# Kernel optimization log

Hardware: AMD Instinct MI355X
Metric: run time of the kernel (lower is better)

Reference implementation:

```python
import jax, jax.numpy as jnp
import numpy as np

D_MODEL = 768; N_LAYERS = 12; D_STATE = 128; D_CONV = 4; HEADDIM = 64
D_INNER = 2 * D_MODEL            # 1536
NHEADS = D_INNER // HEADDIM      # 24
CONV_DIM = D_INNER + 2 * D_STATE # 1792
D_IN_PROJ = 2 * D_INNER + 2 * D_STATE + NHEADS  # 3352
D_FF = 2048; VOCAB = 32000; BATCH = 2; SEQ = 2048
EPS = 1e-5


def setup_inputs() -> dict:
    key = jax.random.key(0)
    ks = jax.random.split(key, 20)
    s = 0.02
    inp = {
        'input_ids': jax.random.randint(ks[0], (BATCH, SEQ), 0, VOCAB),
        'emb':    jax.random.normal(ks[1], (VOCAB, D_MODEL)) * s,
        'ln_w':   jnp.ones((N_LAYERS, D_MODEL)),
        'ln_b':   jnp.zeros((N_LAYERS, D_MODEL)),
        'in_w':   jax.random.normal(ks[2], (N_LAYERS, D_IN_PROJ, D_MODEL)) * s,
        'conv_w': jax.random.normal(ks[3], (N_LAYERS, CONV_DIM, D_CONV)) * 0.1,
        'conv_b': jnp.zeros((N_LAYERS, CONV_DIM)),
        'dt_bias': jax.random.normal(ks[4], (N_LAYERS, NHEADS)) * 0.5,
        'A_log':  jnp.log(1.0 + jax.random.uniform(ks[5], (N_LAYERS, NHEADS)) * 15.0),
        'Dp':     jnp.ones((N_LAYERS, NHEADS)),
        'rms_w':  jnp.ones((N_LAYERS, D_INNER)),
        'out_w':  jax.random.normal(ks[6], (N_LAYERS, D_MODEL, D_INNER)) * s,
        'mlp_ln_w': jnp.ones((N_LAYERS, D_MODEL)),
        'mlp_ln_b': jnp.zeros((N_LAYERS, D_MODEL)),
        'w1':     jax.random.normal(ks[7], (N_LAYERS, D_FF, D_MODEL)) * s,
        'w2':     jax.random.normal(ks[8], (N_LAYERS, D_FF, D_MODEL)) * s,
        'w3':     jax.random.normal(ks[9], (N_LAYERS, D_MODEL, D_FF)) * s,
        'normf_w': jnp.ones((D_MODEL,)),
        'normf_b': jnp.zeros((D_MODEL,)),
        'lm_w':   jax.random.normal(ks[10], (VOCAB, D_MODEL)) * s,
    }
    return inp


def layer_norm(x, w, b):
    mu = jnp.mean(x, -1, keepdims=True)
    xc = x - mu
    var = jnp.mean(xc * xc, -1, keepdims=True)
    return xc * jax.lax.rsqrt(var + EPS) * w + b


def mamba_mixer(h, in_w, conv_w, conv_b, dt_bias, A_log, Dp, rms_w, out_w):
    b, l, _ = h.shape
    zxbcdt = jnp.einsum('bld,ed->ble', h, in_w)                 # [b,l,3352]
    z = zxbcdt[..., :D_INNER]
    xBC = zxbcdt[..., D_INNER:D_INNER + CONV_DIM]
    dt = jax.nn.softplus(zxbcdt[..., D_INNER + CONV_DIM:] + dt_bias)  # [b,l,nh]
    # causal depthwise conv1d over time, kernel D_CONV, then silu
    xpad = jnp.pad(xBC, ((0, 0), (D_CONV - 1, 0), (0, 0)))
    conv = conv_b
    for k in range(D_CONV):
        conv = conv + conv_w[:, k] * xpad[:, k:k + l, :]
    xBC = jax.nn.silu(conv)
    x = xBC[..., :D_INNER].reshape(b, l, NHEADS, HEADDIM)
    Bm = xBC[..., D_INNER:D_INNER + D_STATE]                    # [b,l,n] (ngroups=1)
    Cm = xBC[..., D_INNER + D_STATE:]                           # [b,l,n]
    A = -jnp.exp(A_log)                                         # [nh]
    dA = jnp.exp(dt * A)                                        # [b,l,nh]
    dtB = dt[..., None] * Bm[:, :, None, :]                     # [b,l,nh,n]

    def step(state, inputs):
        dA_t, dtB_t, x_t, C_t = inputs
        state = state * dA_t[..., None, None] + dtB_t[:, :, None, :] * x_t[..., None]
        y_t = jnp.einsum('bhpn,bn->bhp', state, C_t)
        return state, y_t

    state0 = jnp.zeros((b, NHEADS, HEADDIM, D_STATE), dtype=h.dtype)
    xs = (jnp.moveaxis(dA, 1, 0), jnp.moveaxis(dtB, 1, 0),
          jnp.moveaxis(x, 1, 0), jnp.moveaxis(Cm, 1, 0))
    _, ys = jax.lax.scan(step, state0, xs)
    y = jnp.moveaxis(ys, 0, 1) + Dp[None, None, :, None] * x    # [b,l,nh,hd]
    y = y.reshape(b, l, D_INNER)
    # gated RMSNorm (norm_before_gate=False)
    y = y * jax.nn.silu(z)
    y = y * jax.lax.rsqrt(jnp.mean(y * y, -1, keepdims=True) + EPS) * rms_w
    return jnp.einsum('ble,de->bld', y, out_w)


def reference(input_ids, emb, ln_w, ln_b, in_w, conv_w, conv_b, dt_bias, A_log, Dp,
              rms_w, out_w, mlp_ln_w, mlp_ln_b, w1, w2, w3, normf_w, normf_b, lm_w):
    h = emb[input_ids]                                          # [b,l,d]
    for i in range(N_LAYERS):
        resid = h
        hn = layer_norm(resid, ln_w[i], ln_b[i])
        hm = mamba_mixer(hn, in_w[i], conv_w[i], conv_b[i], dt_bias[i],
                         A_log[i], Dp[i], rms_w[i], out_w[i])
        hf = hm + resid
        g = layer_norm(hf, mlp_ln_w[i], mlp_ln_b[i])
        h = hf + jnp.einsum('blf,df->bld', jax.nn.silu(jnp.einsum('bld,fd->blf', g, w1[i])) *
                            jnp.einsum('bld,fd->blf', g, w2[i]), w3[i])
    h = layer_norm(h, normf_w, normf_b)
    return jnp.einsum('bld,vd->blv', h, lm_w)
```

## Files before the change

### kernel.cpp

```cpp
#include <hip/hip_runtime.h>
#include <cstdint>
#include <cstddef>

#define TOK    4096
#define SEQL   2048
#define DMODEL 768
#define NLAYER 12
#define DSTATE 128
#define HEADD  64
#define DINNER 1536
#define NHEADS 24
#define CONVD  1792
#define DIPROJ 3352
#define DIPAD  3456
#define DFF    2048
#define VOCABN 32000
#define NCHUNK 16
#define CHUNKL 128

typedef __attribute__((ext_vector_type(8))) short bf16x8;
typedef __attribute__((ext_vector_type(4))) float f32x4;

__device__ __forceinline__ unsigned short f2bf(float f) {
  union { float f; unsigned u; } v; v.f = f;
  return (unsigned short)((v.u + 0x7FFFu + ((v.u >> 16) & 1u)) >> 16);
}

__device__ __forceinline__ void gld16(const void* g, void* l) {
  __builtin_amdgcn_global_load_lds(
      (const __attribute__((address_space(1))) unsigned int*)g,
      (__attribute__((address_space(3))) unsigned int*)l, 16, 0, 0);
}

__device__ __forceinline__ void stream_store(float* addr, float v) {
  asm volatile("global_store_dword %0, %1, off sc0 sc1 nt" :: "v"(addr), "v"(v) : "memory");
}

template <int NW>
__device__ __forceinline__ void red2t(float& a, float& b) {
#pragma unroll
  for (int o = 1; o < 64; o <<= 1) { a += __shfl_xor(a, o, 64); b += __shfl_xor(b, o, 64); }
  __shared__ float sa[NW], sb[NW];
  const int w = threadIdx.x >> 6;
  if ((threadIdx.x & 63) == 0) { sa[w] = a; sb[w] = b; }
  __syncthreads();
  a = sa[0]; b = sb[0];
#pragma unroll
  for (int i = 1; i < NW; ++i) { a += sa[i]; b += sb[i]; }
}

template <int NW>
__device__ __forceinline__ float red1t(float a) {
#pragma unroll
  for (int o = 1; o < 64; o <<= 1) a += __shfl_xor(a, o, 64);
  __shared__ float sa[NW];
  const int w = threadIdx.x >> 6;
  if ((threadIdx.x & 63) == 0) sa[w] = a;
  __syncthreads();
  float r = sa[0];
#pragma unroll
  for (int i = 1; i < NW; ++i) r += sa[i];
  return r;
}

template <int EPI, int BM, int BN>
__global__ __launch_bounds__(256) void gemm_bt(
    const unsigned short* __restrict__ A, const unsigned short* __restrict__ B,
    float* __restrict__ C, unsigned short* __restrict__ Cg,
    const float* __restrict__ R, int M, int N, int K) {
  constexpr int WM  = BM / 2, WN = BN / 2;
  constexpr int MFR = WM / 16, NFR = WN / 16;
  constexpr int LPS = (BM == 128 ? 2 : 1) + (BN == 128 ? 2 : 1);
  __shared__ unsigned short lA[2][BM * 32];
  __shared__ unsigned short lB[2][BN * 32];

  int lid = (int)blockIdx.x;
  {
    const int nwg = (int)gridDim.x;
    const int xcd = lid & 7;
    const int q = nwg >> 3, r = nwg & 7;
    const int b2 = (xcd < r) ? xcd * (q + 1) : r * (q + 1) + (xcd - r) * q;
    lid = b2 + (lid >> 3);
  }
  const int mtiles = M / BM;
  int m0, n0;
  if constexpr (BM == 128) {
    const int nt = (int)gridDim.x / mtiles;
    const int span = 16 * nt;
    const int g = lid / span, rem = lid % span;
    m0 = (g * 16 + (rem % 16)) * BM;
    n0 = (rem / 16) * BN;
  } else {
    m0 = (lid % mtiles) * BM;
    n0 = (lid / mtiles) * BN;
  }

  const int tid = threadIdx.x, wave = tid >> 6, lane = tid & 63;
  const int wr = (wave >> 1) * WM, wc = (wave & 1) * WN;
  const int srow = lane >> 2;
  const int scol = (((lane & 3) ^ ((lane >> 3) & 3))) * 8;
  const int rdk  = ((lane >> 4) ^ ((lane >> 1) & 3)) * 8;

  f32x4 acc[MFR][NFR];
#pragma unroll
  for (int i = 0; i < MFR; ++i)
#pragma unroll
    for (int j = 0; j < NFR; ++j) acc[i][j] = (f32x4){0.f, 0.f, 0.f, 0.f};

  const size_t arow0 = (size_t)(m0 + (BM == 128 ? wave * 32 : wave * 16) + srow) * K + scol;
  const size_t brow0 = (size_t)(n0 + (BN == 128 ? wave * 32 : wave * 16) + srow) * K + scol;

  auto stage = [&](int buf, int k0) {
    if constexpr (BM == 128) {
      gld16(A + arow0 + k0,                  lA[buf] + (wave * 2 + 0) * 512);
      gld16(A + arow0 + (size_t)16 * K + k0, lA[buf] + (wave * 2 + 1) * 512);
    } else {
      gld16(A + arow0 + k0, lA[buf] + wave * 512);
    }
    if constexpr (BN == 128) {
      gld16(B + brow0 + k0,                  lB[buf] + (wave * 2 + 0) * 512);
      gld16(B + brow0 + (size_t)16 * K + k0, lB[buf] + (wave * 2 + 1) * 512);
    } else {
      gld16(B + brow0 + k0, lB[buf] + wave * 512);
    }
  };

  stage(0, 0);
  stage(1, 32);
  int cur = 0;
  for (int k0 = 0; k0 < K; k0 += 32) {
    asm volatile("s_waitcnt vmcnt(%0)" :: "i"(LPS) : "memory");
    __builtin_amdgcn_s_barrier();
    bf16x8 af[MFR], bfr[NFR];
#pragma unroll
    for (int mi = 0; mi < MFR; ++mi) {
      const int ra = wr + mi * 16 + (lane & 15);
      af[mi] = *(const bf16x8*)&lA[cur][ra * 32 + rdk];
    }
#pragma unroll
    for (int ni = 0; ni < NFR; ++ni) {
      const int rb = wc + ni * 16 + (lane & 15);
      bfr[ni] = *(const bf16x8*)&lB[cur][rb * 32 + rdk];
    }
    asm volatile("s_waitcnt lgkmcnt(0)" ::: "memory");
    __builtin_amdgcn_sched_barrier(0);
    __builtin_amdgcn_s_barrier();
    if (k0 + 64 < K) stage(cur, k0 + 64);
    __builtin_amdgcn_sched_barrier(0);
#pragma unroll
    for (int mi = 0; mi < MFR; ++mi)
#pragma unroll
      for (int ni = 0; ni < NFR; ++ni)
        acc[mi][ni] = __builtin_amdgcn_mfma_f32_16x16x32_bf16(af[mi], bfr[ni], acc[mi][ni], 0, 0, 0);
    cur ^= 1;
  }

  const int er = (lane >> 4) * 4, ec = lane & 15;
#pragma unroll
  for (int mi = 0; mi < MFR; ++mi) {
#pragma unroll
    for (int r = 0; r < 4; ++r) {
      const size_t row = (size_t)(m0 + wr + mi * 16 + er + r);
#pragma unroll
      for (int ni = 0; ni < NFR; ++ni) {
        float v = acc[mi][ni][r];
        const int col = n0 + wc + ec + ni * 16;
        if constexpr (EPI == 2) {
          const float o = __shfl_xor(v, 1, 64);
          if ((lane & 1) == 0)
            Cg[row * DFF + (col >> 1)] = f2bf((v / (1.f + expf(-v))) * o);
        } else if constexpr (EPI == 1) {
          C[row * N + col] = v + R[row * N + col];
        } else if constexpr (EPI == 3) {
          stream_store(&C[row * N + col], v);
        } else {
          C[row * N + col] = v;
        }
      }
    }
  }
}

__global__ __launch_bounds__(256) void cvt_k(const float* __restrict__ in, unsigned short* __restrict__ out, long n) {
  const long i = ((long)blockIdx.x * 256 + threadIdx.x) * 4;
  if (i >= n) return;
  const float4 v = *(const float4*)(in + i);
  ushort4 o; o.x = f2bf(v.x); o.y = f2bf(v.y); o.z = f2bf(v.z); o.w = f2bf(v.w);
  *(ushort4*)(out + i) = o;
}

__global__ __launch_bounds__(256) void cvt_inw_k(const float* __restrict__ in, unsigned short* __restrict__ out) {
  const int row = blockIdx.x;
  const int l = row / DIPAD, n = row % DIPAD;
  unsigned short* orow = out + (size_t)row * DMODEL;
  if (n >= DIPROJ) {
    for (int c = threadIdx.x; c < DMODEL; c += 256) orow[c] = 0;
    return;
  }
  const float* irow = in + ((size_t)l * DIPROJ + n) * DMODEL;
  for (int c = threadIdx.x; c < DMODEL; c += 256) orow[c] = f2bf(irow[c]);
}

__global__ __launch_bounds__(256) void cvt_w12_k(const float* __restrict__ w1, const float* __restrict__ w2,
                                                 unsigned short* __restrict__ out) {
  const int row = blockIdx.x;
  const int l = row / (2 * DFF), rr = row % (2 * DFF);
  const int f = rr >> 1;
  const float* irow = ((rr & 1) == 0) ? (w1 + ((size_t)l * DFF + f) * DMODEL)
                                      : (w2 + ((size_t)l * DFF + f) * DMODEL);
  unsigned short* orow = out + (size_t)row * DMODEL;
  for (int c = threadIdx.x; c < DMODEL; c += 256) orow[c] = f2bf(irow[c]);
}

__global__ __launch_bounds__(192) void embed_k(const int* __restrict__ ids, const float* __restrict__ emb, float* __restrict__ h) {
  const int t = blockIdx.x;
  const float4 v = *(const float4*)(emb + (size_t)ids[t] * DMODEL + threadIdx.x * 4);
  *(float4*)(h + (size_t)t * DMODEL + threadIdx.x * 4) = v;
}

__global__ __launch_bounds__(192) void ln_k(const float* __restrict__ x, const float* __restrict__ w, const float* __restrict__ b,
                                            unsigned short* __restrict__ out) {
  const int t = blockIdx.x, c4 = threadIdx.x * 4;
  const float4 v = *(const float4*)(x + (size_t)t * DMODEL + c4);
  float s = v.x + v.y + v.z + v.w;
  float ss = v.x * v.x + v.y * v.y + v.z * v.z + v.w * v.w;
  red2t<3>(s, ss);
  const float mu = s * (1.f / DMODEL);
  const float inv = rsqrtf(ss * (1.f / DMODEL) - mu * mu + 1e-5f);
  const float4 wv = *(const float4*)(w + c4);
  const float4 bv = *(const float4*)(b + c4);
  ushort4 o;
  o.x = f2bf((v.x - mu) * inv * wv.x + bv.x);
  o.y = f2bf((v.y - mu) * inv * wv.y + bv.y);
  o.z = f2bf((v.z - mu) * inv * wv.z + bv.z);
  o.w = f2bf((v.w - mu) * inv * wv.w + bv.w);
  *(ushort4*)(out + (size_t)t * DMODEL + c4) = o;
}

__global__ __launch_bounds__(448) void conv_k(const float* __restrict__ zx, const float* __restrict__ cw, const float* __restrict__ cb,
                                              const float* __restrict__ dt_bias, const float* __restrict__ A_log,
                                              float* __restrict__ xs, float* __restrict__ Bm, float* __restrict__ Cm,
                                              float* __restrict__ dtv, float* __restrict__ dAv) {
  const int t = blockIdx.x, b = t >> 11, l = t & (SEQL - 1);
  const int c4 = threadIdx.x * 4;
  const float4 w0 = *(const float4*)(cw + c4 * 4);
  const float4 w1v = *(const float4*)(cw + c4 * 4 + 4);
  const float4 w2v = *(const float4*)(cw + c4 * 4 + 8);
  const float4 w3v = *(const float4*)(cw + c4 * 4 + 12);
  float4 a = *(const float4*)(cb + c4);
#pragma unroll
  for (int k = 0; k < 4; ++k) {
    const int ll = l + k - 3;
    if (ll >= 0) {
      const float4 xv = *(const float4*)(zx + (size_t)(b * SEQL + ll) * DIPAD + DINNER + c4);
      a.x = fmaf(((const float*)&w0)[k],  xv.x, a.x);
      a.y = fmaf(((const float*)&w1v)[k], xv.y, a.y);
      a.z = fmaf(((const float*)&w2v)[k], xv.z, a.z);
      a.w = fmaf(((const float*)&w3v)[k], xv.w, a.w);
    }
  }
  a.x = a.x / (1.f + expf(-a.x));
  a.y = a.y / (1.f + expf(-a.y));
  a.z = a.z / (1.f + expf(-a.z));
  a.w = a.w / (1.f + expf(-a.w));
  if (threadIdx.x < 384)      *(float4*)(xs + (size_t)t * DINNER + c4) = a;
  else if (threadIdx.x < 416) *(float4*)(Bm + (size_t)t * DSTATE + (c4 - DINNER)) = a;
  else                        *(float4*)(Cm + (size_t)t * DSTATE + (c4 - DINNER - DSTATE)) = a;
  if (threadIdx.x < NHEADS) {
    const int hh = threadIdx.x;
    const float xv = zx[(size_t)t * DIPAD + DINNER + CONVD + hh] + dt_bias[hh];
    const float dt = (xv > 20.f) ? xv : log1pf(expf(xv));
    dtv[t * NHEADS + hh] = dt;
    dAv[t * NHEADS + hh] = expf(-dt * expf(A_log[hh]));
  }
}

__global__ __launch_bounds__(256) void scan1_k(const float* __restrict__ xs, const float* __restrict__ Bm, const float* __restrict__ Cm,
                                               const float* __restrict__ dtv, const float* __restrict__ dAv,
                                               const float* __restrict__ Dp, float* __restrict__ y,
                                               float* __restrict__ Sloc, float* __restrict__ cumv) {
  __shared__ float lB[2][16][128];
  __shared__ float lC[2][16][128];
  __shared__ float sdA[2][16], sdt[2][16];
  const int pg = blockIdx.x, hh = blockIdx.y, z = blockIdx.z;
  const int b = z >> 4, c = z & (NCHUNK - 1);
  const int pl = threadIdx.x >> 4, ln = threadIdx.x & 15;
  const int p = pg * 16 + pl;
  const int wv = threadIdx.x >> 6, lane = threadIdx.x & 63;
  const float Dph = Dp[hh];
  const int bT = b * SEQL + c * CHUNKL;

  auto stage = [&](int buf, int t0) {
#pragma unroll
    for (int j = 0; j < 2; ++j) {
      const int pr = wv + 4 * j;
      const int row = 2 * pr + (lane >> 5);
      gld16(Bm + (size_t)(t0 + row) * DSTATE + (lane & 31) * 4, &lB[buf][2 * pr][0]);
      gld16(Cm + (size_t)(t0 + row) * DSTATE + (lane & 31) * 4, &lC[buf][2 * pr][0]);
    }
    if (threadIdx.x < 16)      sdA[buf][threadIdx.x]      = dAv[(t0 + threadIdx.x) * NHEADS + hh];
    else if (threadIdx.x < 32) sdt[buf][threadIdx.x - 16] = dtv[(t0 + threadIdx.x - 16) * NHEADS + hh];
  };

  float s0 = 0, s1 = 0, s2 = 0, s3 = 0, s4 = 0, s5 = 0, s6 = 0, s7 = 0;
  float r = 1.f;
  int cur = 0;
  stage(0, bT);
  for (int cc = 0; cc < CHUNKL; cc += 16) {
    const int t0 = bT + cc;
    __builtin_amdgcn_s_barrier();
    float xq[16];
#pragma unroll
    for (int i = 0; i < 16; ++i) xq[i] = xs[(size_t)(t0 + i) * DINNER + hh * HEADD + p];
    if (cc + 16 < CHUNKL) stage(cur ^ 1, t0 + 16);
    asm volatile("s_waitcnt vmcnt(4) lgkmcnt(0)" ::: "memory");
    __builtin_amdgcn_s_barrier();
#pragma unroll
    for (int i = 0; i < 16; ++i) {
      const float dAt = sdA[cur][i], dtt = sdt[cur][i];
      const float xdt = xq[i] * dtt;
      const float4 B0 = *(const float4*)&lB[cur][i][ln * 4];
      const float4 B1 = *(const float4*)&lB[cur][i][64 + ln * 4];
      const float4 C0 = *(const float4*)&lC[cur][i][ln * 4];
      const float4 C1 = *(const float4*)&lC[cur][i][64 + ln * 4];
      float yp;
      s0 = fmaf(s0, dAt, B0.x * xdt); yp = s0 * C0.x;
      s1 = fmaf(s1, dAt, B0.y * xdt); yp = fmaf(s1, C0.y, yp);
      s2 = fmaf(s2, dAt, B0.z * xdt); yp = fmaf(s2, C0.z, yp);
      s3 = fmaf(s3, dAt, B0.w * xdt); yp = fmaf(s3, C0.w, yp);
      s4 = fmaf(s4, dAt, B1.x * xdt); yp = fmaf(s4, C1.x, yp);
      s5 = fmaf(s5, dAt, B1.y * xdt); yp = fmaf(s5, C1.y, yp);
      s6 = fmaf(s6, dAt, B1.z * xdt); yp = fmaf(s6, C1.z, yp);
      s7 = fmaf(s7, dAt, B1.w * xdt); yp = fmaf(s7, C1.w, yp);
#pragma unroll
      for (int o = 1; o < 16; o <<= 1) yp += __shfl_xor(yp, o, 64);
      if (ln == 0) y[(size_t)(t0 + i) * DINNER + hh * HEADD + p] = fmaf(Dph, xq[i], yp);
      r *= dAt;
      if (threadIdx.x == 0) cumv[(size_t)(b * NHEADS + hh) * SEQL + (c * CHUNKL + cc + i)] = r;
    }
    cur ^= 1;
  }
  float* sp = Sloc + (((size_t)(b * NHEADS + hh) * NCHUNK + c) * HEADD + p) * DSTATE;
  *(float4*)(sp + ln * 4)      = (float4){s0, s1, s2, s3};
  *(float4*)(sp + 64 + ln * 4) = (float4){s4, s5, s6, s7};
}

__global__ __launch_bounds__(256) void scan2_k(float* __restrict__ Sloc, const float* __restrict__ cumv) {
  const int bh = blockIdx.x;
  const size_t base = (size_t)bh * NCHUNK * (HEADD * DSTATE);
  const int e0 = threadIdx.x * 32;
  float acc[32];
#pragma unroll
  for (int j = 0; j < 32; ++j) acc[j] = 0.f;
  for (int c = 1; c < NCHUNK; ++c) {
    const float Pc = cumv[(size_t)bh * SEQL + c * CHUNKL - 1];
    float* slot = Sloc + base + (size_t)(c - 1) * (HEADD * DSTATE) + e0;
#pragma unroll
    for (int j = 0; j < 32; j += 4) {
      const float4 sl = *(const float4*)(slot + j);
      acc[j]     = fmaf(Pc, acc[j],     sl.x);
      acc[j + 1] = fmaf(Pc, acc[j + 1], sl.y);
      acc[j + 2] = fmaf(Pc, acc[j + 2], sl.z);
      acc[j + 3] = fmaf(Pc, acc[j + 3], sl.w);
      *(float4*)(slot + j) = (float4){acc[j], acc[j + 1], acc[j + 2], acc[j + 3]};
    }
  }
}

__global__ __launch_bounds__(256) void scan3_k(const float* __restrict__ Cm, const float* __restrict__ cumv,
                                               const float* __restrict__ Sloc, float* __restrict__ y) {
  __shared__ float lC[2][16][128];
  __shared__ float sCum[2][16];
  const int pg = blockIdx.x, hh = blockIdx.y, z = blockIdx.z;
  const int b = z / (NCHUNK - 1), c = z % (NCHUNK - 1) + 1;
  const int pl = threadIdx.x >> 4, ln = threadIdx.x & 15;
  const int p = pg * 16 + pl;
  const int wv = threadIdx.x >> 6, lane = threadIdx.x & 63;
  const int bT = b * SEQL + c * CHUNKL;
  const float* sp = Sloc + (((size_t)(b * NHEADS + hh) * NCHUNK + (c - 1)) * HEADD + p) * DSTATE;
  const float4 sA = *(const float4*)(sp + ln * 4);
  const float4 sB = *(const float4*)(sp + 64 + ln * 4);

  auto stage = [&](int buf, int t0) {
#pragma unroll
    for (int j = 0; j < 2; ++j) {
      const int pr = wv + 4 * j;
      const int row = 2 * pr + (lane >> 5);
      gld16(Cm + (size_t)(t0 + row) * DSTATE + (lane & 31) * 4, &lC[buf][2 * pr][0]);
    }
    if (threadIdx.x < 16)
      sCum[buf][threadIdx.x] = cumv[(size_t)(b * NHEADS + hh) * SEQL + (t0 - b * SEQL) + threadIdx.x];
  };

  int cur = 0;
  stage(0, bT);
  for (int cc = 0; cc < CHUNKL; cc += 16) {
    const int t0 = bT + cc;
    __builtin_amdgcn_s_barrier();
    float yq[16];
#pragma unroll
    for (int i = 0; i < 16; ++i) yq[i] = y[(size_t)(t0 + i) * DINNER + hh * HEADD + p];
    if (cc + 16 < CHUNKL) stage(cur ^ 1, t0 + 16);
    asm volatile("s_waitcnt vmcnt(2) lgkmcnt(0)" ::: "memory");
    __builtin_amdgcn_s_barrier();
#pragma unroll
    for (int i = 0; i < 16; ++i) {
      const float4 C0 = *(const float4*)&lC[cur][i][ln * 4];
      const float4 C1 = *(const float4*)&lC[cur][i][64 + ln * 4];
      float yp = sA.x * C0.x;
      yp = fmaf(sA.y, C0.y, yp);
      yp = fmaf(sA.z, C0.z, yp);
      yp = fmaf(sA.w, C0.w, yp);
      yp = fmaf(sB.x, C1.x, yp);
      yp = fmaf(sB.y, C1.y, yp);
      yp = fmaf(sB.z, C1.z, yp);
      yp = fmaf(sB.w, C1.w, yp);
#pragma unroll
      for (int o = 1; o < 16; o <<= 1) yp += __shfl_xor(yp, o, 64);
      if (ln == 0) y[(size_t)(t0 + i) * DINNER + hh * HEADD + p] = fmaf(sCum[cur][i], yp, yq[i]);
    }
    cur ^= 1;
  }
}

__global__ __launch_bounds__(384) void grms_k(const float* __restrict__ y, const float* __restrict__ zx,
                                              const float* __restrict__ rw, unsigned short* __restrict__ out) {
  const int t = blockIdx.x, c4 = threadIdx.x * 4;
  const float4 yv = *(const float4*)(y + (size_t)t * DINNER + c4);
  const float4 zv = *(const float4*)(zx + (size_t)t * DIPAD + c4);
  float4 g;
  g.x = yv.x * (zv.x / (1.f + expf(-zv.x)));
  g.y = yv.y * (zv.y / (1.f + expf(-zv.y)));
  g.z = yv.z * (zv.z / (1.f + expf(-zv.z)));
  g.w = yv.w * (zv.w / (1.f + expf(-zv.w)));
  float ss = g.x * g.x + g.y * g.y + g.z * g.z + g.w * g.w;
  ss = red1t<6>(ss);
  const float inv = rsqrtf(ss * (1.f / DINNER) + 1e-5f);
  const float4 rv = *(const float4*)(rw + c4);
  ushort4 o;
  o.x = f2bf(g.x * inv * rv.x);
  o.y = f2bf(g.y * inv * rv.y);
  o.z = f2bf(g.z * inv * rv.z);
  o.w = f2bf(g.w * inv * rv.w);
  *(ushort4*)(out + (size_t)t * DINNER + c4) = o;
}

extern "C" void kernel_launch(void* const* d_in, const int* in_sizes, int n_in,
                              void* d_out, int out_size, void* d_ws, size_t ws_size,
                              hipStream_t stream) {
  const int*   ids      = (const int*)  d_in[0];
  const float* emb      = (const float*)d_in[1];
  const float* ln_w     = (const float*)d_in[2];
  const float* ln_b     = (const float*)d_in[3];
  const float* in_w     = (const float*)d_in[4];
  const float* conv_w   = (const float*)d_in[5];
  const float* conv_b   = (const float*)d_in[6];
  const float* dt_bias  = (const float*)d_in[7];
  const float* A_log    = (const float*)d_in[8];
  const float* Dp       = (const float*)d_in[9];
  const float* rms_w    = (const float*)d_in[10];
  const float* out_w    = (const float*)d_in[11];
  const float* mlp_ln_w = (const float*)d_in[12];
  const float* mlp_ln_b = (const float*)d_in[13];
  const float* w1       = (const float*)d_in[14];
  const float* w2       = (const float*)d_in[15];
  const float* w3       = (const float*)d_in[16];
  const float* normf_w  = (const float*)d_in[17];
  const float* normf_b  = (const float*)d_in[18];
  const float* lm_w     = (const float*)d_in[19];

  char* base = (char*)d_ws;
  size_t off = 0;
  auto alloc = [&](size_t bytes) -> char* {
    char* p = base + off;
    off += (bytes + 255) & ~(size_t)255;
    return p;
  };
  float* h             = (float*)alloc((size_t)TOK * DMODEL * 4);
  unsigned short* xn   = (unsigned short*)alloc((size_t)TOK * DMODEL * 2);
  float* zx            = (float*)alloc((size_t)TOK * DIPAD * 4);
  float* xs            = (float*)alloc((size_t)TOK * DINNER * 4);
  float* Bm            = (float*)alloc((size_t)TOK * DSTATE * 4);
  float* Cm            = (float*)alloc((size_t)TOK * DSTATE * 4);
  float* dtv           = (float*)alloc((size_t)TOK * NHEADS * 4);
  float* dAv           = (float*)alloc((size_t)TOK * NHEADS * 4);
  float* y             = (float*)alloc((size_t)TOK * DINNER * 4);
  unsigned short* ybf  = (unsigned short*)alloc((size_t)TOK * DINNER * 2);
  float* hf            = (float*)alloc((size_t)TOK * DMODEL * 4);
  unsigned short* gbf  = (unsigned short*)alloc((size_t)TOK * DMODEL * 2);
  unsigned short* gate = (unsigned short*)alloc((size_t)TOK * DFF * 2);
  float* Sloc          = (float*)alloc((size_t)2 * NHEADS * NCHUNK * HEADD * DSTATE * 4);
  float* cumv          = (float*)alloc((size_t)2 * NHEADS * SEQL * 4);
  unsigned short* inw_bf  = (unsigned short*)alloc((size_t)NLAYER * DIPAD * DMODEL * 2);
  unsigned short* outw_bf = (unsigned short*)alloc((size_t)NLAYER * DMODEL * DINNER * 2);
  unsigned short* w12_bf  = (unsigned short*)alloc((size_t)NLAYER * 2 * DFF * DMODEL * 2);
  unsigned short* w3_bf   = (unsigned short*)alloc((size_t)NLAYER * DMODEL * DFF * 2);
  unsigned short* lm_bf   = (unsigned short*)alloc((size_t)VOCABN * DMODEL * 2);
  if (off > ws_size) return;

  cvt_inw_k<<<NLAYER * DIPAD, 256, 0, stream>>>(in_w, inw_bf);
  cvt_w12_k<<<NLAYER * 2 * DFF, 256, 0, stream>>>(w1, w2, w12_bf);
  {
    const long n1 = (long)NLAYER * DMODEL * DINNER;
    cvt_k<<<(unsigned)((n1 + 1023) / 1024), 256, 0, stream>>>(out_w, outw_bf, n1);
    const long n3 = (long)NLAYER * DMODEL * DFF;
    cvt_k<<<(unsigned)((n3 + 1023) / 1024), 256, 0, stream>>>(w3, w3_bf, n3);
    const long n4 = (long)VOCABN * DMODEL;
    cvt_k<<<(unsigned)((n4 + 1023) / 1024), 256, 0, stream>>>(lm_w, lm_bf, n4);
  }

  embed_k<<<TOK, 192, 0, stream>>>(ids, emb, h);

  for (int l = 0; l < NLAYER; ++l) {
    ln_k<<<TOK, 192, 0, stream>>>(h, ln_w + l * DMODEL, ln_b + l * DMODEL, xn);
    gemm_bt<0, 128, 128><<<(TOK / 128) * (DIPAD / 128), 256, 0, stream>>>(
        xn, inw_bf + (size_t)l * DIPAD * DMODEL, zx, nullptr, nullptr, TOK, DIPAD, DMODEL);
    conv_k<<<TOK, 448, 0, stream>>>(zx, conv_w + (size_t)l * CONVD * 4, conv_b + (size_t)l * CONVD,
                                    dt_bias + l * NHEADS, A_log + l * NHEADS, xs, Bm, Cm, dtv, dAv);
    scan1_k<<<dim3(4, NHEADS, 2 * NCHUNK), 256, 0, stream>>>(xs, Bm, Cm, dtv, dAv, Dp + l * NHEADS, y, Sloc, cumv);
    scan2_k<<<2 * NHEADS, 256, 0, stream>>>(Sloc, cumv);
    scan3_k<<<dim3(4, NHEADS, 2 * (NCHUNK - 1)), 256, 0, stream>>>(Cm, cumv, Sloc, y);
    grms_k<<<TOK, 384, 0, stream>>>(y, zx, rms_w + (size_t)l * DINNER, ybf);
    gemm_bt<1, 64, 64><<<(TOK / 64) * (DMODEL / 64), 256, 0, stream>>>(
        ybf, outw_bf + (size_t)l * DMODEL * DINNER, hf, nullptr, h, TOK, DMODEL, DINNER);
    ln_k<<<TOK, 192, 0, stream>>>(hf, mlp_ln_w + l * DMODEL, mlp_ln_b + l * DMODEL, gbf);
    gemm_bt<2, 128, 128><<<(TOK / 128) * (2 * DFF / 128), 256, 0, stream>>>(
        gbf, w12_bf + (size_t)l * 2 * DFF * DMODEL, nullptr, gate, nullptr, TOK, 2 * DFF, DMODEL);
    gemm_bt<1, 64, 64><<<(TOK / 64) * (DMODEL / 64), 256, 0, stream>>>(
        gate, w3_bf + (size_t)l * DMODEL * DFF, h, nullptr, hf, TOK, DMODEL, DFF);
  }

  ln_k<<<TOK, 192, 0, stream>>>(h, normf_w, normf_b, xn);
  gemm_bt<3, 128, 128><<<(TOK / 128) * (VOCABN / 128), 256, 0, stream>>>(
      xn, lm_bf, (float*)d_out, nullptr, nullptr, TOK, VOCABN, DMODEL);
}
```

Measured before the change: 6.645 ms.

## Enlarge GEMM tiles to 256x128 and fold chunk-state scan into scan3

Adds a 256-row tile variant to the bf16 GEMM and uses it for the in-proj, gate/up and LM-head GEMMs, while the out-proj and down-proj GEMMs move from 64x64 to 128x64 tiles. The aim is more operand reuse per block and fewer blocks. It also removes the separate scan2 kernel: each scan3 block now rebuilds its inter-chunk state by looping over the earlier chunk states itself. That saves one launch per layer but adds redundant reads of Sloc that grow with chunk index. A launch_bounds occupancy hint of 2 is added, which may constrain registers for the larger tiles.

```diff
diff --git a/kernel.cpp b/kernel.cpp
--- a/kernel.cpp
+++ b/kernel.cpp
@@ -64,13 +64,13 @@
 }
 
 template <int EPI, int BM, int BN>
-__global__ __launch_bounds__(256) void gemm_bt(
+__global__ __launch_bounds__(256, 2) void gemm_bt(
     const unsigned short* __restrict__ A, const unsigned short* __restrict__ B,
     float* __restrict__ C, unsigned short* __restrict__ Cg,
     const float* __restrict__ R, int M, int N, int K) {
   constexpr int WM  = BM / 2, WN = BN / 2;
   constexpr int MFR = WM / 16, NFR = WN / 16;
-  constexpr int LPS = (BM == 128 ? 2 : 1) + (BN == 128 ? 2 : 1);
+  constexpr int LPS = (BM == 256 ? 4 : BM == 128 ? 2 : 1) + (BN == 128 ? 2 : 1);
   __shared__ unsigned short lA[2][BM * 32];
   __shared__ unsigned short lB[2][BN * 32];
 
@@ -84,12 +84,13 @@
   }
   const int mtiles = M / BM;
   int m0, n0;
-  if constexpr (BM == 128) {
+  if constexpr (BM >= 128 && BN == 128) {
+    constexpr int GRP = (BM == 256) ? 8 : 16;
     const int nt = (int)gridDim.x / mtiles;
-    const int span = 16 * nt;
+    const int span = GRP * nt;
     const int g = lid / span, rem = lid % span;
-    m0 = (g * 16 + (rem % 16)) * BM;
-    n0 = (rem / 16) * BN;
+    m0 = (g * GRP + (rem % GRP)) * BM;
+    n0 = (rem / GRP) * BN;
   } else {
     m0 = (lid % mtiles) * BM;
     n0 = (lid / mtiles) * BN;
@@ -107,11 +108,15 @@
 #pragma unroll
     for (int j = 0; j < NFR; ++j) acc[i][j] = (f32x4){0.f, 0.f, 0.f, 0.f};
 
-  const size_t arow0 = (size_t)(m0 + (BM == 128 ? wave * 32 : wave * 16) + srow) * K + scol;
+  const size_t arow0 = (size_t)(m0 + (BM == 256 ? wave * 64 : BM == 128 ? wave * 32 : wave * 16) + srow) * K + scol;
   const size_t brow0 = (size_t)(n0 + (BN == 128 ? wave * 32 : wave * 16) + srow) * K + scol;
 
   auto stage = [&](int buf, int k0) {
-    if constexpr (BM == 128) {
+    if constexpr (BM == 256) {
+#pragma unroll
+      for (int j = 0; j < 4; ++j)
+        gld16(A + arow0 + (size_t)(j * 16) * K + k0, lA[buf] + (wave * 4 + j) * 512);
+    } else if constexpr (BM == 128) {
       gld16(A + arow0 + k0,                  lA[buf] + (wave * 2 + 0) * 512);
       gld16(A + arow0 + (size_t)16 * K + k0, lA[buf] + (wave * 2 + 1) * 512);
     } else {
@@ -345,28 +350,6 @@
   *(float4*)(sp + 64 + ln * 4) = (float4){s4, s5, s6, s7};
 }
 
-__global__ __launch_bounds__(256) void scan2_k(float* __restrict__ Sloc, const float* __restrict__ cumv) {
-  const int bh = blockIdx.x;
-  const size_t base = (size_t)bh * NCHUNK * (HEADD * DSTATE);
-  const int e0 = threadIdx.x * 32;
-  float acc[32];
-#pragma unroll
-  for (int j = 0; j < 32; ++j) acc[j] = 0.f;
-  for (int c = 1; c < NCHUNK; ++c) {
-    const float Pc = cumv[(size_t)bh * SEQL + c * CHUNKL - 1];
-    float* slot = Sloc + base + (size_t)(c - 1) * (HEADD * DSTATE) + e0;
-#pragma unroll
-    for (int j = 0; j < 32; j += 4) {
-      const float4 sl = *(const float4*)(slot + j);
-      acc[j]     = fmaf(Pc, acc[j],     sl.x);
-      acc[j + 1] = fmaf(Pc, acc[j + 1], sl.y);
-      acc[j + 2] = fmaf(Pc, acc[j + 2], sl.z);
-      acc[j + 3] = fmaf(Pc, acc[j + 3], sl.w);
-      *(float4*)(slot + j) = (float4){acc[j], acc[j + 1], acc[j + 2], acc[j + 3]};
-    }
-  }
-}
-
 __global__ __launch_bounds__(256) void scan3_k(const float* __restrict__ Cm, const float* __restrict__ cumv,
                                                const float* __restrict__ Sloc, float* __restrict__ y) {
   __shared__ float lC[2][16][128];
@@ -377,9 +360,21 @@
   const int p = pg * 16 + pl;
   const int wv = threadIdx.x >> 6, lane = threadIdx.x & 63;
   const int bT = b * SEQL + c * CHUNKL;
-  const float* sp = Sloc + (((size_t)(b * NHEADS + hh) * NCHUNK + (c - 1)) * HEADD + p) * DSTATE;
-  const float4 sA = *(const float4*)(sp + ln * 4);
-  const float4 sB = *(const float4*)(sp + 64 + ln * 4);
+
+  float4 sA = (float4){0.f, 0.f, 0.f, 0.f}, sB = (float4){0.f, 0.f, 0.f, 0.f};
+  {
+    const float* spb = Sloc + ((size_t)(b * NHEADS + hh) * NCHUNK) * (HEADD * DSTATE) + (size_t)p * DSTATE;
+    for (int j = 1; j <= c; ++j) {
+      const float Pj = cumv[(size_t)(b * NHEADS + hh) * SEQL + j * CHUNKL - 1];
+      const float* sj = spb + (size_t)(j - 1) * (HEADD * DSTATE);
+      const float4 v0 = *(const float4*)(sj + ln * 4);
+      const float4 v1 = *(const float4*)(sj + 64 + ln * 4);
+      sA.x = fmaf(Pj, sA.x, v0.x); sA.y = fmaf(Pj, sA.y, v0.y);
+      sA.z = fmaf(Pj, sA.z, v0.z); sA.w = fmaf(Pj, sA.w, v0.w);
+      sB.x = fmaf(Pj, sB.x, v1.x); sB.y = fmaf(Pj, sB.y, v1.y);
+      sB.z = fmaf(Pj, sB.z, v1.z); sB.w = fmaf(Pj, sB.w, v1.w);
+    }
+  }
 
   auto stage = [&](int buf, int t0) {
 #pragma unroll
@@ -513,24 +508,23 @@
 
   for (int l = 0; l < NLAYER; ++l) {
     ln_k<<<TOK, 192, 0, stream>>>(h, ln_w + l * DMODEL, ln_b + l * DMODEL, xn);
-    gemm_bt<0, 128, 128><<<(TOK / 128) * (DIPAD / 128), 256, 0, stream>>>(
+    gemm_bt<0, 256, 128><<<(TOK / 256) * (DIPAD / 128), 256, 0, stream>>>(
         xn, inw_bf + (size_t)l * DIPAD * DMODEL, zx, nullptr, nullptr, TOK, DIPAD, DMODEL);
     conv_k<<<TOK, 448, 0, stream>>>(zx, conv_w + (size_t)l * CONVD * 4, conv_b + (size_t)l * CONVD,
                                     dt_bias + l * NHEADS, A_log + l * NHEADS, xs, Bm, Cm, dtv, dAv);
     scan1_k<<<dim3(4, NHEADS, 2 * NCHUNK), 256, 0, stream>>>(xs, Bm, Cm, dtv, dAv, Dp + l * NHEADS, y, Sloc, cumv);
-    scan2_k<<<2 * NHEADS, 256, 0, stream>>>(Sloc, cumv);
     scan3_k<<<dim3(4, NHEADS, 2 * (NCHUNK - 1)), 256, 0, stream>>>(Cm, cumv, Sloc, y);
     grms_k<<<TOK, 384, 0, stream>>>(y, zx, rms_w + (size_t)l * DINNER, ybf);
-    gemm_bt<1, 64, 64><<<(TOK / 64) * (DMODEL / 64), 256, 0, stream>>>(
+    gemm_bt<1, 128, 64><<<(TOK / 128) * (DMODEL / 64), 256, 0, stream>>>(
         ybf, outw_bf + (size_t)l * DMODEL * DINNER, hf, nullptr, h, TOK, DMODEL, DINNER);
     ln_k<<<TOK, 192, 0, stream>>>(hf, mlp_ln_w + l * DMODEL, mlp_ln_b + l * DMODEL, gbf);
-    gemm_bt<2, 128, 128><<<(TOK / 128) * (2 * DFF / 128), 256, 0, stream>>>(
+    gemm_bt<2, 256, 128><<<(TOK / 256) * (2 * DFF / 128), 256, 0, stream>>>(
         gbf, w12_bf + (size_t)l * 2 * DFF * DMODEL, nullptr, gate, nullptr, TOK, 2 * DFF, DMODEL);
-    gemm_bt<1, 64, 64><<<(TOK / 64) * (DMODEL / 64), 256, 0, stream>>>(
+    gemm_bt<1, 128, 64><<<(TOK / 128) * (DMODEL / 64), 256, 0, stream>>>(
         gate, w3_bf + (size_t)l * DMODEL * DFF, h, nullptr, hf, TOK, DMODEL, DFF);
   }
 
   ln_k<<<TOK, 192, 0, stream>>>(h, normf_w, normf_b, xn);
-  gemm_bt<3, 128, 128><<<(TOK / 128) * (VOCABN / 128), 256, 0, stream>>>(
+  gemm_bt<3, 256, 128><<<(TOK / 256) * (VOCABN / 128), 256, 0, stream>>>(
       xn, lm_bf, (float*)d_out, nullptr, nullptr, TOK, VOCABN, DMODEL);
 }
```

Result: faster. 5.955 ms (-10.4%).
